# Kernel optimization log

Hardware: AMD Instinct MI355X
Metric: run time of the kernel (lower is better)

Reference implementation:

```python
import jax, jax.numpy as jnp
import numpy as np

N_NODES = 50000
E = 800000
D = 64
H = 128


def _ln(x, g, b, eps=1e-5):
    m = x.mean(-1, keepdims=True)
    v = ((x - m) ** 2).mean(-1, keepdims=True)
    return (x - m) * jax.lax.rsqrt(v + eps) * g + b


def setup_inputs() -> dict:
    key = jax.random.key(0)
    ks = jax.random.split(key, 8)
    return dict(
        node_emb=jax.random.normal(ks[0], (N_NODES, D), jnp.float32),
        src=jax.random.randint(ks[1], (E,), 0, N_NODES),
        dst=jax.random.randint(ks[2], (E,), 0, N_NODES),
        noise=jax.random.uniform(ks[3], (E,), jnp.float32, 1e-6, 1.0 - 1e-6),
        W1=jax.random.normal(ks[4], (2 * D, H), jnp.float32) * 0.05,
        b1=jnp.zeros((H,), jnp.float32),
        g1=jnp.ones((H,), jnp.float32),
        bt1=jnp.zeros((H,), jnp.float32),
        W2=jax.random.normal(ks[5], (H, H // 2), jnp.float32) * 0.05,
        b2=jnp.zeros((H // 2,), jnp.float32),
        g2=jnp.ones((H // 2,), jnp.float32),
        bt2=jnp.zeros((H // 2,), jnp.float32),
        W3=jax.random.normal(ks[6], (H // 2, 1), jnp.float32) * 0.05,
        b3=jnp.zeros((1,), jnp.float32),
    )


def reference(node_emb, src, dst, noise, W1, b1, g1, bt1, W2, b2, g2, bt2, W3, b3):
    # edge gather + concat: [E, 2D]
    edge_emb = jnp.concatenate([node_emb[src], node_emb[dst]], axis=1)
    # edge MLP with LayerNorm + relu (dropout=0 / eval)
    h = jax.nn.relu(_ln(edge_emb @ W1 + b1, g1, bt1))
    h = jax.nn.relu(_ln(h @ W2 + b2, g2, bt2))
    logit = (h @ W3 + b3).reshape(-1)  # [E]
    # concrete gate, bias=0, beta=1.0 (forward default)
    beta = 1.0
    gate = jax.nn.sigmoid((jnp.log(noise) - jnp.log1p(-noise) + logit) / beta)
    # degree norm: out_deg(src)^-1/2 * in_deg(dst)^-1/2, degrees clamped to >=1
    ones = jnp.ones((src.shape[0],), node_emb.dtype)
    out_deg = jnp.maximum(jax.ops.segment_sum(ones, src, num_segments=N_NODES), 1.0)
    in_deg = jnp.maximum(jax.ops.segment_sum(ones, dst, num_segments=N_NODES), 1.0)
    norm = jax.lax.rsqrt(out_deg)[src] * jax.lax.rsqrt(in_deg)[dst]
    return gate * norm
```

## Files before the change

kernel.cpp:

```cpp
#include <hip/hip_runtime.h>
#include <hip/hip_bf16.h>

#define N_NODES 50000
#define NE      800000
#define NT16    (NE / 16)
#define NTILES  (NE / 16)

typedef __attribute__((ext_vector_type(8)))  short bf16x8;
typedef __attribute__((ext_vector_type(4)))  float f32x4;
typedef __attribute__((ext_vector_type(4)))  int   i32x4;
typedef __attribute__((ext_vector_type(2)))  int   i32x2;

static __device__ __forceinline__ short f2bf(float x) {
    union { float f; unsigned u; } v; v.f = x;
    unsigned r = (v.u + 0x7fffu + ((v.u >> 16) & 1u)) >> 16;
    return (short)r;
}
static __device__ __forceinline__ float bflo(unsigned u) {
    union { unsigned u; float f; } v; v.u = u << 16; return v.f;
}
static __device__ __forceinline__ float bfhi(unsigned u) {
    union { unsigned u; float f; } v; v.u = u & 0xffff0000u; return v.f;
}
static __device__ __forceinline__ unsigned pk2bf(float a, float b) {
    union { __hip_bfloat162 h; unsigned u; } v;
    float2 f; f.x = a; f.y = b;
    v.h = __float22bfloat162_rn(f);
    return v.u;
}

#define OFF_W2   32768
#define OFF_B1   49152
#define OFF_B2   49408
#define OFF_GT1  49536
#define OFF_GT2  50048
#define OFF_W3   50304
#define IMG_B    50432
#define IMG_V4   (IMG_B / 16)


__global__ void prep_hist(const float* __restrict__ emb,
                          const int* __restrict__ src, const int* __restrict__ dst,
                          const float* __restrict__ W1, const float* __restrict__ b1,
                          const float* __restrict__ g1, const float* __restrict__ bt1,
                          const float* __restrict__ W2, const float* __restrict__ b2,
                          const float* __restrict__ g2, const float* __restrict__ bt2,
                          const float* __restrict__ W3,
                          ushort* __restrict__ embB, char* __restrict__ img,
                          int* __restrict__ outd, int* __restrict__ ind)
{
    const int i0 = blockIdx.x * 256 + threadIdx.x;
    const int n  = gridDim.x * 256;

    for (int t = i0; t < (N_NODES * 64 / 8); t += n) {
        const f32x4* p = (const f32x4*)(emb + (size_t)t * 8);
        f32x4 a = p[0], b = p[1];
        unsigned u0 = pk2bf(a[0], a[1]);
        unsigned u1 = pk2bf(a[2], a[3]);
        unsigned u2 = pk2bf(b[0], b[1]);
        unsigned u3 = pk2bf(b[2], b[3]);
        i32x4 o = {(int)u0, (int)u1, (int)u2, (int)u3};
        *(i32x4*)(embB + (size_t)t * 8) = o;
    }
    for (int t = i0; t < NE / 4; t += n) {
        i32x4 s4 = ((const i32x4*)src)[t];
        i32x4 d4 = ((const i32x4*)dst)[t];
        atomicAdd(outd + s4[0], 1); atomicAdd(outd + s4[1], 1);
        atomicAdd(outd + s4[2], 1); atomicAdd(outd + s4[3], 1);
        atomicAdd(ind + d4[0], 1); atomicAdd(ind + d4[1], 1);
        atomicAdd(ind + d4[2], 1); atomicAdd(ind + d4[3], 1);
    }
    ushort* W1f = (ushort*)img;
    for (int t = i0; t < 16384; t += n) {
        int j = t & 7, lane = (t >> 3) & 63, f = t >> 9;
        int tt = f >> 2, ks = f & 3, g = lane >> 4, c = lane & 15;
        W1f[t] = f2bf(W1[(ks * 32 + g * 8 + j) * 128 + tt * 16 + c]);
    }
    ushort* W2f = (ushort*)(img + OFF_W2);
    for (int t = i0; t < 8192; t += n) {
        int j = t & 7, lane = (t >> 3) & 63, f = t >> 9;
        int t2 = f >> 2, ks = f & 3, g = lane >> 4, c = lane & 15;
        W2f[t] = f2bf(W2[(ks * 32 + g * 8 + j) * 64 + t2 * 16 + c]);
    }
    if (i0 < 128) ((ushort*)(img + OFF_B1))[i0] = f2bf(b1[i0]);
    if (i0 < 64)  ((ushort*)(img + OFF_B2))[i0] = f2bf(b2[i0]);
    if (i0 < 128)
        ((unsigned*)(img + OFF_GT1))[i0] =
            (unsigned)(ushort)f2bf(g1[i0]) | ((unsigned)(ushort)f2bf(bt1[i0]) << 16);
    if (i0 < 64) {
        ((unsigned*)(img + OFF_GT2))[i0] =
            (unsigned)(ushort)f2bf(g2[i0]) | ((unsigned)(ushort)f2bf(bt2[i0]) << 16);
        ((ushort*)(img + OFF_W3))[i0] = f2bf(W3[i0]);
    }
}


__global__ __launch_bounds__(256, 3) void edge_mlp16(
    const ushort* __restrict__ embB,
    const int*   __restrict__ src, const int* __restrict__ dst,
    const float* __restrict__ noise,
    const i32x4* __restrict__ WFimg,
    const float* __restrict__ b3p,
    const int* __restrict__ outd, const int* __restrict__ ind,
    float* __restrict__ out)
{
    __shared__ i32x4 ldsv[IMG_V4];
    char* ldsb = (char*)ldsv;

    const int tid = threadIdx.x;
    for (int i = tid; i < IMG_V4; i += 256) ldsv[i] = WFimg[i];
    __syncthreads();

    const int l = tid & 63;
    const int g = l >> 4;
    const int c = l & 15;

    const float b3v = b3p[0];

    bf16x8 bone = {};
    bone[0] = (g == 0) ? (short)0x3F80 : (short)0;

    const int addrA = (((g & 1) * 2) * 16 + c) * 4;
    const int addrB = addrA + 64;

    const int gw = blockIdx.x * 4 + (tid >> 6);
    const int nw = gridDim.x * 4;

    int sn, dn;
    bf16x8 fS0, fS1, fD0, fD1;
    {
        int t0 = (gw < NT16) ? gw : (NT16 - 1);
        int e0p = t0 * 16 + c;
        sn = src[e0p]; dn = dst[e0p];
        const ushort* sp = embB + (size_t)sn * 64;
        const ushort* dp = embB + (size_t)dn * 64;
        fS0 = *(const bf16x8*)(sp + g * 8);
        fS1 = *(const bf16x8*)(sp + 32 + g * 8);
        fD0 = *(const bf16x8*)(dp + g * 8);
        fD1 = *(const bf16x8*)(dp + 32 + g * 8);
    }

    for (int tile = gw; tile < NT16; tile += nw) {
        unsigned tz;
        asm volatile("v_mov_b32 %0, 0" : "=v"(tz));
        const char* ldz = ldsb + tz;

        const int e0 = tile * 16 + c;

        const int tn  = tile + nw;
        const int tcl = (tn < NT16) ? tn : tile;
        const int e0n = tcl * 16 + c;
        int snN = src[e0n];
        int dnN = dst[e0n];
        float nz = noise[e0];
        int odv = outd[sn];
        int idv = ind[dn];

        const ushort* W1z = (const ushort*)ldz;
        f32x4 acc1[8] = {};
#pragma unroll
        for (int ks = 0; ks < 4; ++ks) {
            bf16x8 bf = (ks == 0) ? fS0 : (ks == 1) ? fS1 : (ks == 2) ? fD0 : fD1;
#pragma unroll
            for (int t = 0; t < 8; ++t) {
                bf16x8 w = *(const bf16x8*)(W1z + (t * 4 + ks) * 512 + l * 8);
                acc1[t] = __builtin_amdgcn_mfma_f32_16x16x32_bf16(w, bf, acc1[t], 0, 0, 0);
            }
        }
        const ushort* b1z = (const ushort*)(ldz + OFF_B1);
#pragma unroll
        for (int t = 0; t < 8; ++t) {
            bf16x8 w = {};
            short bv = b1z[t * 16 + c];
            w[0] = (g == 0) ? bv : (short)0;
            acc1[t] = __builtin_amdgcn_mfma_f32_16x16x32_bf16(w, bone, acc1[t], 0, 0, 0);
        }

        float s0 = 0.f, s1 = 0.f, q0 = 0.f, q1 = 0.f;
#pragma unroll
        for (int t = 0; t < 8; ++t) {
            float v0 = acc1[t][0], v1 = acc1[t][1], v2 = acc1[t][2], v3 = acc1[t][3];
            s0 += v0 + v2; q0 = fmaf(v0, v0, fmaf(v2, v2, q0));
            s1 += v1 + v3; q1 = fmaf(v1, v1, fmaf(v3, v3, q1));
        }
        float s = s0 + s1, q = q0 + q1;
        s += __shfl_xor(s, 16); s += __shfl_xor(s, 32);
        q += __shfl_xor(q, 16); q += __shfl_xor(q, 32);
        const float mu = s * (1.0f / 128.0f);
        const float rs = rsqrtf(q * (1.0f / 128.0f) - mu * mu + 1e-5f);
        const float c0 = -mu * rs;

        unsigned pku[8][2];
#pragma unroll
        for (int t = 0; t < 8; ++t) {
            i32x4 pg = *(const i32x4*)(ldz + OFF_GT1 + t * 64 + g * 16);
            float y0, y1, y2, y3;
            {
                float w0 = fmaf(acc1[t][0], rs, c0);
                y0 = fmaxf(fmaf(w0, bflo((unsigned)pg[0]), bfhi((unsigned)pg[0])), 0.f);
                float w1 = fmaf(acc1[t][1], rs, c0);
                y1 = fmaxf(fmaf(w1, bflo((unsigned)pg[1]), bfhi((unsigned)pg[1])), 0.f);
                float w2 = fmaf(acc1[t][2], rs, c0);
                y2 = fmaxf(fmaf(w2, bflo((unsigned)pg[2]), bfhi((unsigned)pg[2])), 0.f);
                float w3 = fmaf(acc1[t][3], rs, c0);
                y3 = fmaxf(fmaf(w3, bflo((unsigned)pg[3]), bfhi((unsigned)pg[3])), 0.f);
            }
            pku[t][0] = pk2bf(y0, y1);
            pku[t][1] = pk2bf(y2, y3);
        }

        const ushort* W2z = (const ushort*)(ldz + OFF_W2);
        f32x4 acc2[4] = {};
#pragma unroll
        for (int ks = 0; ks < 4; ++ks) {
            int a0 = __builtin_amdgcn_ds_bpermute(addrA, (int)pku[2 * ks][0]);
            int b0 = __builtin_amdgcn_ds_bpermute(addrA, (int)pku[2 * ks + 1][0]);
            int a1 = __builtin_amdgcn_ds_bpermute(addrA, (int)pku[2 * ks][1]);
            int b1_ = __builtin_amdgcn_ds_bpermute(addrA, (int)pku[2 * ks + 1][1]);
            int a2 = __builtin_amdgcn_ds_bpermute(addrB, (int)pku[2 * ks][0]);
            int b2_ = __builtin_amdgcn_ds_bpermute(addrB, (int)pku[2 * ks + 1][0]);
            int a3 = __builtin_amdgcn_ds_bpermute(addrB, (int)pku[2 * ks][1]);
            int b3_ = __builtin_amdgcn_ds_bpermute(addrB, (int)pku[2 * ks + 1][1]);
            union { i32x4 i; bf16x8 b; } u;
            u.i[0] = (g & 2) ? b0 : a0;
            u.i[1] = (g & 2) ? b1_ : a1;
            u.i[2] = (g & 2) ? b2_ : a2;
            u.i[3] = (g & 2) ? b3_ : a3;
#pragma unroll
            for (int t2 = 0; t2 < 4; ++t2) {
                bf16x8 w = *(const bf16x8*)(W2z + (t2 * 4 + ks) * 512 + l * 8);
                acc2[t2] = __builtin_amdgcn_mfma_f32_16x16x32_bf16(w, u.b, acc2[t2], 0, 0, 0);
            }
        }
        const ushort* b2z = (const ushort*)(ldz + OFF_B2);
#pragma unroll
        for (int t2 = 0; t2 < 4; ++t2) {
            bf16x8 w = {};
            short bv = b2z[t2 * 16 + c];
            w[0] = (g == 0) ? bv : (short)0;
            acc2[t2] = __builtin_amdgcn_mfma_f32_16x16x32_bf16(w, bone, acc2[t2], 0, 0, 0);
        }

        {
            const ushort* spn = embB + (size_t)snN * 64;
            const ushort* dpn = embB + (size_t)dnN * 64;
            fS0 = *(const bf16x8*)(spn + g * 8);
            fS1 = *(const bf16x8*)(spn + 32 + g * 8);
            fD0 = *(const bf16x8*)(dpn + g * 8);
            fD1 = *(const bf16x8*)(dpn + 32 + g * 8);
        }

        float t0 = 0.f, t1 = 0.f, p0 = 0.f, p1 = 0.f;
#pragma unroll
        for (int t2 = 0; t2 < 4; ++t2) {
            float v0 = acc2[t2][0], v1 = acc2[t2][1], v2 = acc2[t2][2], v3 = acc2[t2][3];
            t0 += v0 + v2; p0 = fmaf(v0, v0, fmaf(v2, v2, p0));
            t1 += v1 + v3; p1 = fmaf(v1, v1, fmaf(v3, v3, p1));
        }
        float s2 = t0 + t1, q2 = p0 + p1;
        s2 += __shfl_xor(s2, 16); s2 += __shfl_xor(s2, 32);
        q2 += __shfl_xor(q2, 16); q2 += __shfl_xor(q2, 32);
        const float mu2 = s2 * (1.0f / 64.0f);
        const float rs2 = rsqrtf(q2 * (1.0f / 64.0f) - mu2 * mu2 + 1e-5f);
        const float c02 = -mu2 * rs2;

        float lg = 0.f;
#pragma unroll
        for (int t2 = 0; t2 < 4; ++t2) {
            i32x4 pg = *(const i32x4*)(ldz + OFF_GT2 + t2 * 64 + g * 16);
            i32x2 wq = *(const i32x2*)(ldz + OFF_W3 + t2 * 32 + g * 8);
#pragma unroll
            for (int r = 0; r < 4; ++r) {
                unsigned ug = (unsigned)pg[r];
                unsigned wu = (unsigned)wq[r >> 1];
                float w3v = (r & 1) ? bfhi(wu) : bflo(wu);
                float w = fmaf(acc2[t2][r], rs2, c02);
                float y = fmaxf(fmaf(w, bflo(ug), bfhi(ug)), 0.f);
                lg = fmaf(y, w3v, lg);
            }
        }
        lg += __shfl_xor(lg, 16);
        lg += __shfl_xor(lg, 32);
        lg += b3v;

        if (g == 0) {
            float z = __logf(nz) - log1pf(-nz) + lg;
            float gate = 1.0f / (1.0f + __expf(-z));
            int od = odv; if (od < 1) od = 1;
            int idg = idv; if (idg < 1) idg = 1;
            out[e0] = gate * (rsqrtf((float)od) * rsqrtf((float)idg));
        }

        sn = snN; dn = dnN;
    }
}


__global__ void degree_hist(const int* __restrict__ src, const int* __restrict__ dst,
                            int* __restrict__ outd, int* __restrict__ ind) {
    int i = blockIdx.x * 256 + threadIdx.x;
    if (i < NE) {
        atomicAdd(outd + src[i], 1);
        atomicAdd(ind + dst[i], 1);
    }
}

__global__ __launch_bounds__(256, 2) void edge_mlp_mfma(
    const float* __restrict__ emb,
    const int*   __restrict__ src, const int* __restrict__ dst,
    const float* __restrict__ noise,
    const float* __restrict__ W1, const float* __restrict__ b1,
    const float* __restrict__ g1, const float* __restrict__ bt1,
    const float* __restrict__ W2, const float* __restrict__ b2,
    const float* __restrict__ g2, const float* __restrict__ bt2,
    const float* __restrict__ W3, const float* __restrict__ b3,
    const int*   __restrict__ outd, const int* __restrict__ ind,
    float* __restrict__ out)
{
    __shared__ short lds[32768];
    const int tid = threadIdx.x;
    const int wid = tid >> 6;
    const int l   = tid & 63;
    const int g   = l >> 4;
    const int c   = l & 15;

    for (int i = tid; i < 16384; i += 256) {
        int j = i & 7, lane = (i >> 3) & 63, p = i >> 9;
        int ks = p >> 3, t = p & 7;
        int row = ks * 32 + (lane >> 4) * 8 + j;
        int col = t * 16 + (lane & 15);
        lds[i] = f2bf(W1[row * 128 + col]);
    }
    for (int i = tid; i < 8192; i += 256) {
        int j = i & 7, lane = (i >> 3) & 63, p = i >> 9;
        int ks = p >> 2, t = p & 3;
        int row = ks * 32 + (lane >> 4) * 8 + j;
        int col = t * 16 + (lane & 15);
        lds[16384 + i] = f2bf(W2[row * 64 + col]);
    }
    __syncthreads();

    short* Hl = lds + 24576 + wid * 2048;
    float b1v[8], g1v[8], t1v[8];
#pragma unroll
    for (int t = 0; t < 8; ++t) { int f = t * 16 + c; b1v[t] = b1[f]; g1v[t] = g1[f]; t1v[t] = bt1[f]; }
    float b2v[4], g2v[4], t2v[4], w3v[4];
#pragma unroll
    for (int t = 0; t < 4; ++t) { int f = t * 16 + c; b2v[t] = b2[f]; g2v[t] = g2[f]; t2v[t] = bt2[f]; w3v[t] = W3[f]; }
    const float b3v = b3[0];

    const int gw = blockIdx.x * 4 + wid;
    const int nw = gridDim.x * 4;

    for (int tile = gw; tile < NTILES; tile += nw) {
        const int e0 = tile * 16 + c;
        const int sn = src[e0], dn = dst[e0];
        const f32x4* sp = (const f32x4*)(emb + (size_t)sn * 64);
        const f32x4* dp = (const f32x4*)(emb + (size_t)dn * 64);
        f32x4 u[8];
        u[0] = sp[2 * g]; u[1] = sp[2 * g + 1];
        u[2] = sp[8 + 2 * g]; u[3] = sp[8 + 2 * g + 1];
        u[4] = dp[2 * g]; u[5] = dp[2 * g + 1];
        u[6] = dp[8 + 2 * g]; u[7] = dp[8 + 2 * g + 1];

        bf16x8 a1[4];
#pragma unroll
        for (int ks = 0; ks < 4; ++ks) {
            f32x4 x0 = u[2 * ks], x1 = u[2 * ks + 1];
            bf16x8 a;
            a[0] = f2bf(x0[0]); a[1] = f2bf(x0[1]); a[2] = f2bf(x0[2]); a[3] = f2bf(x0[3]);
            a[4] = f2bf(x1[0]); a[5] = f2bf(x1[1]); a[6] = f2bf(x1[2]); a[7] = f2bf(x1[3]);
            a1[ks] = a;
        }
        f32x4 acc1[8];
#pragma unroll
        for (int t = 0; t < 8; ++t) { f32x4 z = {b1v[t], b1v[t], b1v[t], b1v[t]}; acc1[t] = z; }
#pragma unroll
        for (int ks = 0; ks < 4; ++ks) {
#pragma unroll
            for (int t = 0; t < 8; ++t) {
                bf16x8 b = *(const bf16x8*)(lds + (ks * 8 + t) * 512 + l * 8);
                acc1[t] = __builtin_amdgcn_mfma_f32_16x16x32_bf16(a1[ks], b, acc1[t], 0, 0, 0);
            }
        }
        float mean[4], rstd[4];
#pragma unroll
        for (int r = 0; r < 4; ++r) {
            float s = acc1[0][r];
#pragma unroll
            for (int t = 1; t < 8; ++t) s += acc1[t][r];
            s += __shfl_xor(s, 1); s += __shfl_xor(s, 2);
            s += __shfl_xor(s, 4); s += __shfl_xor(s, 8);
            float m = s * (1.0f / 128.0f);
            float q = 0.f;
#pragma unroll
            for (int t = 0; t < 8; ++t) { float d = acc1[t][r] - m; q = fmaf(d, d, q); }
            q += __shfl_xor(q, 1); q += __shfl_xor(q, 2);
            q += __shfl_xor(q, 4); q += __shfl_xor(q, 8);
            mean[r] = m; rstd[r] = rsqrtf(q * (1.0f / 128.0f) + 1e-5f);
        }
#pragma unroll
        for (int r = 0; r < 4; ++r) {
            int rw = g * 4 + r;
            int swz = (rw & 7) << 3;
#pragma unroll
            for (int t = 0; t < 8; ++t) {
                float y = fmaf((acc1[t][r] - mean[r]) * rstd[r], g1v[t], t1v[t]);
                y = fmaxf(y, 0.f);
                Hl[rw * 128 + ((t * 16 + c) ^ swz)] = f2bf(y);
            }
        }
        bf16x8 a2[4];
        const int swzr = (c & 7) << 3;
#pragma unroll
        for (int ks = 0; ks < 4; ++ks)
            a2[ks] = *(const bf16x8*)(Hl + c * 128 + ((ks * 32 + g * 8) ^ swzr));

        f32x4 acc2[4];
#pragma unroll
        for (int t = 0; t < 4; ++t) { f32x4 z = {b2v[t], b2v[t], b2v[t], b2v[t]}; acc2[t] = z; }
#pragma unroll
        for (int ks = 0; ks < 4; ++ks) {
#pragma unroll
            for (int t = 0; t < 4; ++t) {
                bf16x8 b = *(const bf16x8*)(lds + 16384 + (ks * 4 + t) * 512 + l * 8);
                acc2[t] = __builtin_amdgcn_mfma_f32_16x16x32_bf16(a2[ks], b, acc2[t], 0, 0, 0);
            }
        }
        float logit[4];
#pragma unroll
        for (int r = 0; r < 4; ++r) {
            float s = acc2[0][r] + acc2[1][r] + acc2[2][r] + acc2[3][r];
            s += __shfl_xor(s, 1); s += __shfl_xor(s, 2);
            s += __shfl_xor(s, 4); s += __shfl_xor(s, 8);
            float m = s * (1.0f / 64.0f);
            float q = 0.f;
#pragma unroll
            for (int t = 0; t < 4; ++t) { float d = acc2[t][r] - m; q = fmaf(d, d, q); }
            q += __shfl_xor(q, 1); q += __shfl_xor(q, 2);
            q += __shfl_xor(q, 4); q += __shfl_xor(q, 8);
            float rs = rsqrtf(q * (1.0f / 64.0f) + 1e-5f);
            float p = 0.f;
#pragma unroll
            for (int t = 0; t < 4; ++t) {
                float y = fmaf((acc2[t][r] - m) * rs, g2v[t], t2v[t]);
                y = fmaxf(y, 0.f);
                p = fmaf(y, w3v[t], p);
            }
            p += __shfl_xor(p, 1); p += __shfl_xor(p, 2);
            p += __shfl_xor(p, 4); p += __shfl_xor(p, 8);
            logit[r] = p + b3v;
        }
        if (c < 4) {
            int e = tile * 16 + g * 4 + c;
            float lg = (c == 0) ? logit[0] : (c == 1) ? logit[1] : (c == 2) ? logit[2] : logit[3];
            float nz = noise[e];
            float z = __logf(nz) - log1pf(-nz) + lg;
            float gate = 1.0f / (1.0f + __expf(-z));
            int od = outd[src[e]]; if (od < 1) od = 1;
            int idg = ind[dst[e]]; if (idg < 1) idg = 1;
            out[e] = gate * (rsqrtf((float)od) * rsqrtf((float)idg));
        }
    }
}


extern "C" void kernel_launch(void* const* d_in, const int* in_sizes, int n_in,
                              void* d_out, int out_size, void* d_ws, size_t ws_size,
                              hipStream_t stream) {
    const float* emb   = (const float*)d_in[0];
    const int*   src   = (const int*)  d_in[1];
    const int*   dst   = (const int*)  d_in[2];
    const float* noise = (const float*)d_in[3];
    const float* W1  = (const float*)d_in[4];
    const float* b1  = (const float*)d_in[5];
    const float* g1  = (const float*)d_in[6];
    const float* bt1 = (const float*)d_in[7];
    const float* W2  = (const float*)d_in[8];
    const float* b2  = (const float*)d_in[9];
    const float* g2  = (const float*)d_in[10];
    const float* bt2 = (const float*)d_in[11];
    const float* W3  = (const float*)d_in[12];
    const float* b3  = (const float*)d_in[13];

    char* ws = (char*)d_ws;
    const size_t NEED = 6400000 + IMG_B + 400000;

    if (ws_size >= NEED) {
        ushort* embB = (ushort*)ws;
        char*   img  = ws + 6400000;
        int* outd = (int*)(ws + 6400000 + IMG_B);
        int* ind  = outd + N_NODES;

        hipMemsetAsync(outd, 0, 2 * N_NODES * sizeof(int), stream);
        prep_hist<<<2048, 256, 0, stream>>>(emb, src, dst, W1, b1, g1, bt1,
                                            W2, b2, g2, bt2, W3,
                                            embB, img, outd, ind);
        edge_mlp16<<<1536, 256, 0, stream>>>(embB, src, dst, noise, (const i32x4*)img,
                                             b3, outd, ind, (float*)d_out);
    } else {
        int* outd = (int*)ws;
        int* ind  = outd + N_NODES;
        hipMemsetAsync(outd, 0, 2 * N_NODES * sizeof(int), stream);
        degree_hist<<<(NE + 255) / 256, 256, 0, stream>>>(src, dst, outd, ind);
        edge_mlp_mfma<<<512, 256, 0, stream>>>(emb, src, dst, noise,
                                               W1, b1, g1, bt1,
                                               W2, b2, g2, bt2,
                                               W3, b3, outd, ind,
                                               (float*)d_out);
    }
}
```

Measured before the change: 172.2 us.

## Precompute per-node first-layer projections and gather them per edge

Splits the first linear layer algebraically: each node's embedding is projected once by the source and destination halves of W1 in a new node-level MFMA GEMM kernel, with half the bias folded into each half. The edge kernel then gathers two 128-wide bf16 projection rows per edge and adds them, replacing the per-edge 128x128 matmul. The ds_bpermute shuffle is also replaced with xor shuffles. This removes most of the edge-level first-layer MFMA work and shrinks the LDS image to raise occupancy, but per-edge gather traffic roughly doubles (512 bytes per edge instead of 256) and a separate kernel launch plus a 25.6 MB intermediate buffer are added.

New measurement: 188.3 us. 9.4% more time.

```diff
diff --git a/kernel.cpp b/kernel.cpp
--- a/kernel.cpp
+++ b/kernel.cpp
@@ -8,6 +8,7 @@
 
 typedef __attribute__((ext_vector_type(8)))  short bf16x8;
 typedef __attribute__((ext_vector_type(4)))  float f32x4;
+typedef __attribute__((ext_vector_type(16))) float f32x16;
 typedef __attribute__((ext_vector_type(4)))  int   i32x4;
 typedef __attribute__((ext_vector_type(2)))  int   i32x2;
 
@@ -29,39 +30,38 @@
     return v.u;
 }
 
-#define OFF_W2   32768
-#define OFF_B1   49152
-#define OFF_B2   49408
-#define OFF_GT1  49536
-#define OFF_GT2  50048
-#define OFF_W3   50304
-#define IMG_B    50432
-#define IMG_V4   (IMG_B / 16)
-
-
-__global__ void prep_hist(const float* __restrict__ emb,
-                          const int* __restrict__ src, const int* __restrict__ dst,
-                          const float* __restrict__ W1, const float* __restrict__ b1,
-                          const float* __restrict__ g1, const float* __restrict__ bt1,
-                          const float* __restrict__ W2, const float* __restrict__ b2,
-                          const float* __restrict__ g2, const float* __restrict__ bt2,
-                          const float* __restrict__ W3,
-                          ushort* __restrict__ embB, char* __restrict__ img,
-                          int* __restrict__ outd, int* __restrict__ ind)
+#define GOFF_BH  32768
+#define GIMG_B   33280
+#define GIMG_V4  (GIMG_B / 16)
+
+#define I2_B2    16384
+#define I2_GT1   16512
+#define I2_GT2   17024
+#define I2_W3    17280
+#define IMG2_B   17408
+#define IMG2_V4  (IMG2_B / 16)
+
+#define WS_P     0
+#define WS_GIMG  25600000
+#define WS_IMG2  25633280
+#define WS_OUTD  25650688
+#define WS_IND   25850688
+#define WS_NEED  26050688
+
+
+__global__ void prep_all(const float* __restrict__ emb,
+                         const int* __restrict__ src, const int* __restrict__ dst,
+                         const float* __restrict__ W1, const float* __restrict__ b1,
+                         const float* __restrict__ g1, const float* __restrict__ bt1,
+                         const float* __restrict__ W2, const float* __restrict__ b2,
+                         const float* __restrict__ g2, const float* __restrict__ bt2,
+                         const float* __restrict__ W3,
+                         char* __restrict__ gimg, char* __restrict__ img2,
+                         int* __restrict__ outd, int* __restrict__ ind)
 {
     const int i0 = blockIdx.x * 256 + threadIdx.x;
     const int n  = gridDim.x * 256;
 
-    for (int t = i0; t < (N_NODES * 64 / 8); t += n) {
-        const f32x4* p = (const f32x4*)(emb + (size_t)t * 8);
-        f32x4 a = p[0], b = p[1];
-        unsigned u0 = pk2bf(a[0], a[1]);
-        unsigned u1 = pk2bf(a[2], a[3]);
-        unsigned u2 = pk2bf(b[0], b[1]);
-        unsigned u3 = pk2bf(b[2], b[3]);
-        i32x4 o = {(int)u0, (int)u1, (int)u2, (int)u3};
-        *(i32x4*)(embB + (size_t)t * 8) = o;
-    }
     for (int t = i0; t < NE / 4; t += n) {
         i32x4 s4 = ((const i32x4*)src)[t];
         i32x4 d4 = ((const i32x4*)dst)[t];
@@ -70,45 +70,117 @@
         atomicAdd(ind + d4[0], 1); atomicAdd(ind + d4[1], 1);
         atomicAdd(ind + d4[2], 1); atomicAdd(ind + d4[3], 1);
     }
-    ushort* W1f = (ushort*)img;
+    ushort* W1f = (ushort*)gimg;
     for (int t = i0; t < 16384; t += n) {
         int j = t & 7, lane = (t >> 3) & 63, f = t >> 9;
-        int tt = f >> 2, ks = f & 3, g = lane >> 4, c = lane & 15;
-        W1f[t] = f2bf(W1[(ks * 32 + g * 8 + j) * 128 + tt * 16 + c]);
-    }
-    ushort* W2f = (ushort*)(img + OFF_W2);
+        int ft = f >> 2, ks = f & 3, h = lane >> 5, cc = lane & 31;
+        int k = 16 * ks + 8 * h + j;
+        int fo = 32 * ft + cc;
+        float v = (fo < 128) ? W1[k * 128 + fo] : W1[(64 + k) * 128 + (fo - 128)];
+        W1f[t] = f2bf(v);
+    }
+    if (i0 < 256) ((ushort*)(gimg + GOFF_BH))[i0] = f2bf(0.5f * b1[i0 & 127]);
+
+    ushort* W2f = (ushort*)img2;
     for (int t = i0; t < 8192; t += n) {
         int j = t & 7, lane = (t >> 3) & 63, f = t >> 9;
         int t2 = f >> 2, ks = f & 3, g = lane >> 4, c = lane & 15;
         W2f[t] = f2bf(W2[(ks * 32 + g * 8 + j) * 64 + t2 * 16 + c]);
     }
-    if (i0 < 128) ((ushort*)(img + OFF_B1))[i0] = f2bf(b1[i0]);
-    if (i0 < 64)  ((ushort*)(img + OFF_B2))[i0] = f2bf(b2[i0]);
+    if (i0 < 64)  ((ushort*)(img2 + I2_B2))[i0] = f2bf(b2[i0]);
     if (i0 < 128)
-        ((unsigned*)(img + OFF_GT1))[i0] =
+        ((unsigned*)(img2 + I2_GT1))[i0] =
             (unsigned)(ushort)f2bf(g1[i0]) | ((unsigned)(ushort)f2bf(bt1[i0]) << 16);
     if (i0 < 64) {
-        ((unsigned*)(img + OFF_GT2))[i0] =
+        ((unsigned*)(img2 + I2_GT2))[i0] =
             (unsigned)(ushort)f2bf(g2[i0]) | ((unsigned)(ushort)f2bf(bt2[i0]) << 16);
-        ((ushort*)(img + OFF_W3))[i0] = f2bf(W3[i0]);
-    }
-}
-
-
-__global__ __launch_bounds__(256, 3) void edge_mlp16(
-    const ushort* __restrict__ embB,
+        ((ushort*)(img2 + I2_W3))[i0] = f2bf(W3[i0]);
+    }
+}
+
+
+#define NT_NODE 1563
+
+__global__ __launch_bounds__(256, 2) void gemm_P(
+    const float* __restrict__ emb, const i32x4* __restrict__ GIMG,
+    ushort* __restrict__ P)
+{
+    __shared__ i32x4 ldsg[GIMG_V4];
+    char* gb = (char*)ldsg;
+    const int tid = threadIdx.x;
+    for (int i = tid; i < GIMG_V4; i += 256) ldsg[i] = GIMG[i];
+    __syncthreads();
+
+    const int l = tid & 63;
+    const int h = l >> 5;
+    const int c = l & 31;
+
+    bf16x8 bone = {};
+    bone[0] = (h == 0) ? (short)0x3F80 : (short)0;
+
+    const ushort* W1z = (const ushort*)gb;
+    const ushort* bhz = (const ushort*)(gb + GOFF_BH);
+
+    const int gw = blockIdx.x * 4 + (tid >> 6);
+    const int nw = gridDim.x * 4;
+    const int NTT = NT_NODE * 8;
+
+    for (int tt = gw; tt < NTT; tt += nw) {
+        const int nt = tt >> 3;
+        const int ft = tt & 7;
+        const int nn = nt * 32 + c;
+        const int ncl = (nn < N_NODES) ? nn : (N_NODES - 1);
+        const float* er = emb + (size_t)ncl * 64;
+
+        f32x16 acc = {};
+#pragma unroll
+        for (int ks = 0; ks < 4; ++ks) {
+            f32x4 x0 = *(const f32x4*)(er + 16 * ks + 8 * h);
+            f32x4 x1 = *(const f32x4*)(er + 16 * ks + 8 * h + 4);
+            bf16x8 bf;
+            bf[0] = f2bf(x0[0]); bf[1] = f2bf(x0[1]); bf[2] = f2bf(x0[2]); bf[3] = f2bf(x0[3]);
+            bf[4] = f2bf(x1[0]); bf[5] = f2bf(x1[1]); bf[6] = f2bf(x1[2]); bf[7] = f2bf(x1[3]);
+            bf16x8 w = *(const bf16x8*)(W1z + (ft * 4 + ks) * 512 + l * 8);
+            acc = __builtin_amdgcn_mfma_f32_32x32x16_bf16(w, bf, acc, 0, 0, 0);
+        }
+        {
+            bf16x8 w = {};
+            short bv = (short)bhz[32 * ft + c];
+            w[0] = (h == 0) ? bv : (short)0;
+            acc = __builtin_amdgcn_mfma_f32_32x32x16_bf16(w, bone, acc, 0, 0, 0);
+        }
+        if (nn < N_NODES) {
+#pragma unroll
+            for (int q = 0; q < 4; ++q) {
+                int fl = 8 * q + 4 * h;
+                int f  = 32 * ft + fl;
+                int fh = f & 127, half = f >> 7;
+                int t  = fh >> 4, gg = (fh >> 2) & 3;
+                ushort* dp = P + (size_t)nn * 256 + half * 128 + gg * 32 + t * 4;
+                i32x2 o;
+                o[0] = (int)pk2bf(acc[4 * q],     acc[4 * q + 1]);
+                o[1] = (int)pk2bf(acc[4 * q + 2], acc[4 * q + 3]);
+                *(i32x2*)dp = o;
+            }
+        }
+    }
+}
+
+
+__global__ __launch_bounds__(256, 4) void edge_mlp_p(
+    const ushort* __restrict__ P,
     const int*   __restrict__ src, const int* __restrict__ dst,
     const float* __restrict__ noise,
-    const i32x4* __restrict__ WFimg,
+    const i32x4* __restrict__ IMG2,
     const float* __restrict__ b3p,
     const int* __restrict__ outd, const int* __restrict__ ind,
     float* __restrict__ out)
 {
-    __shared__ i32x4 ldsv[IMG_V4];
+    __shared__ i32x4 ldsv[IMG2_V4];
     char* ldsb = (char*)ldsv;
 
     const int tid = threadIdx.x;
-    for (int i = tid; i < IMG_V4; i += 256) ldsv[i] = WFimg[i];
+    for (int i = tid; i < IMG2_V4; i += 256) ldsv[i] = IMG2[i];
     __syncthreads();
 
     const int l = tid & 63;
@@ -120,24 +192,19 @@
     bf16x8 bone = {};
     bone[0] = (g == 0) ? (short)0x3F80 : (short)0;
 
-    const int addrA = (((g & 1) * 2) * 16 + c) * 4;
-    const int addrB = addrA + 64;
-
     const int gw = blockIdx.x * 4 + (tid >> 6);
     const int nw = gridDim.x * 4;
 
     int sn, dn;
-    bf16x8 fS0, fS1, fD0, fD1;
+    i32x4 ps0, ps1, ps2, ps3, pd0, pd1, pd2, pd3;
     {
         int t0 = (gw < NT16) ? gw : (NT16 - 1);
         int e0p = t0 * 16 + c;
         sn = src[e0p]; dn = dst[e0p];
-        const ushort* sp = embB + (size_t)sn * 64;
-        const ushort* dp = embB + (size_t)dn * 64;
-        fS0 = *(const bf16x8*)(sp + g * 8);
-        fS1 = *(const bf16x8*)(sp + 32 + g * 8);
-        fD0 = *(const bf16x8*)(dp + g * 8);
-        fD1 = *(const bf16x8*)(dp + 32 + g * 8);
+        const i32x4* sp = (const i32x4*)(P + (size_t)sn * 256 + g * 32);
+        const i32x4* dp = (const i32x4*)(P + (size_t)dn * 256 + 128 + g * 32);
+        ps0 = sp[0]; ps1 = sp[1]; ps2 = sp[2]; ps3 = sp[3];
+        pd0 = dp[0]; pd1 = dp[1]; pd2 = dp[2]; pd3 = dp[3];
     }
 
     for (int tile = gw; tile < NT16; tile += nw) {
@@ -156,34 +223,22 @@
         int odv = outd[sn];
         int idv = ind[dn];
 
-        const ushort* W1z = (const ushort*)ldz;
-        f32x4 acc1[8] = {};
-#pragma unroll
-        for (int ks = 0; ks < 4; ++ks) {
-            bf16x8 bf = (ks == 0) ? fS0 : (ks == 1) ? fS1 : (ks == 2) ? fD0 : fD1;
-#pragma unroll
-            for (int t = 0; t < 8; ++t) {
-                bf16x8 w = *(const bf16x8*)(W1z + (t * 4 + ks) * 512 + l * 8);
-                acc1[t] = __builtin_amdgcn_mfma_f32_16x16x32_bf16(w, bf, acc1[t], 0, 0, 0);
-            }
-        }
-        const ushort* b1z = (const ushort*)(ldz + OFF_B1);
-#pragma unroll
-        for (int t = 0; t < 8; ++t) {
-            bf16x8 w = {};
-            short bv = b1z[t * 16 + c];
-            w[0] = (g == 0) ? bv : (short)0;
-            acc1[t] = __builtin_amdgcn_mfma_f32_16x16x32_bf16(w, bone, acc1[t], 0, 0, 0);
-        }
-
-        float s0 = 0.f, s1 = 0.f, q0 = 0.f, q1 = 0.f;
-#pragma unroll
-        for (int t = 0; t < 8; ++t) {
-            float v0 = acc1[t][0], v1 = acc1[t][1], v2 = acc1[t][2], v3 = acc1[t][3];
-            s0 += v0 + v2; q0 = fmaf(v0, v0, fmaf(v2, v2, q0));
-            s1 += v1 + v3; q1 = fmaf(v1, v1, fmaf(v3, v3, q1));
-        }
-        float s = s0 + s1, q = q0 + q1;
+        float s = 0.f, q = 0.f;
+        {
+            i32x4 pcs[4] = {ps0, ps1, ps2, ps3};
+            i32x4 pcd[4] = {pd0, pd1, pd2, pd3};
+#pragma unroll
+            for (int i = 0; i < 4; ++i) {
+#pragma unroll
+                for (int w = 0; w < 4; ++w) {
+                    unsigned sv = (unsigned)pcs[i][w], dv = (unsigned)pcd[i][w];
+                    float a = bflo(sv) + bflo(dv);
+                    float b = bfhi(sv) + bfhi(dv);
+                    s += a + b;
+                    q = fmaf(a, a, fmaf(b, b, q));
+                }
+            }
+        }
         s += __shfl_xor(s, 16); s += __shfl_xor(s, 32);
         q += __shfl_xor(q, 16); q += __shfl_xor(q, 32);
         const float mu = s * (1.0f / 128.0f);
@@ -191,73 +246,80 @@
         const float c0 = -mu * rs;
 
         unsigned pku[8][2];
-#pragma unroll
-        for (int t = 0; t < 8; ++t) {
-            i32x4 pg = *(const i32x4*)(ldz + OFF_GT1 + t * 64 + g * 16);
-            float y0, y1, y2, y3;
-            {
-                float w0 = fmaf(acc1[t][0], rs, c0);
-                y0 = fmaxf(fmaf(w0, bflo((unsigned)pg[0]), bfhi((unsigned)pg[0])), 0.f);
-                float w1 = fmaf(acc1[t][1], rs, c0);
-                y1 = fmaxf(fmaf(w1, bflo((unsigned)pg[1]), bfhi((unsigned)pg[1])), 0.f);
-                float w2 = fmaf(acc1[t][2], rs, c0);
-                y2 = fmaxf(fmaf(w2, bflo((unsigned)pg[2]), bfhi((unsigned)pg[2])), 0.f);
-                float w3 = fmaf(acc1[t][3], rs, c0);
-                y3 = fmaxf(fmaf(w3, bflo((unsigned)pg[3]), bfhi((unsigned)pg[3])), 0.f);
-            }
-            pku[t][0] = pk2bf(y0, y1);
-            pku[t][1] = pk2bf(y2, y3);
-        }
-
-        const ushort* W2z = (const ushort*)(ldz + OFF_W2);
+        {
+            i32x4 pcs[4] = {ps0, ps1, ps2, ps3};
+            i32x4 pcd[4] = {pd0, pd1, pd2, pd3};
+#pragma unroll
+            for (int t = 0; t < 8; ++t) {
+                i32x4 pg = *(const i32x4*)(ldz + I2_GT1 + t * 64 + g * 16);
+                unsigned sv0 = (unsigned)pcs[t >> 1][(t & 1) * 2];
+                unsigned sv1 = (unsigned)pcs[t >> 1][(t & 1) * 2 + 1];
+                unsigned dv0 = (unsigned)pcd[t >> 1][(t & 1) * 2];
+                unsigned dv1 = (unsigned)pcd[t >> 1][(t & 1) * 2 + 1];
+                float h0 = bflo(sv0) + bflo(dv0);
+                float h1_ = bfhi(sv0) + bfhi(dv0);
+                float h2 = bflo(sv1) + bflo(dv1);
+                float h3 = bfhi(sv1) + bfhi(dv1);
+                float y0 = fmaxf(fmaf(fmaf(h0, rs, c0), bflo((unsigned)pg[0]), bfhi((unsigned)pg[0])), 0.f);
+                float y1 = fmaxf(fmaf(fmaf(h1_, rs, c0), bflo((unsigned)pg[1]), bfhi((unsigned)pg[1])), 0.f);
+                float y2 = fmaxf(fmaf(fmaf(h2, rs, c0), bflo((unsigned)pg[2]), bfhi((unsigned)pg[2])), 0.f);
+                float y3 = fmaxf(fmaf(fmaf(h3, rs, c0), bflo((unsigned)pg[3]), bfhi((unsigned)pg[3])), 0.f);
+                pku[t][0] = pk2bf(y0, y1);
+                pku[t][1] = pk2bf(y2, y3);
+            }
+        }
+
+        {
+            const i32x4* sp = (const i32x4*)(P + (size_t)snN * 256 + g * 32);
+            const i32x4* dp = (const i32x4*)(P + (size_t)dnN * 256 + 128 + g * 32);
+            ps0 = sp[0]; ps1 = sp[1]; ps2 = sp[2]; ps3 = sp[3];
+            pd0 = dp[0]; pd1 = dp[1]; pd2 = dp[2]; pd3 = dp[3];
+        }
+
+        const ushort* W2z = (const ushort*)ldz;
         f32x4 acc2[4] = {};
+        const bool gh = (g & 2) != 0;
+        const bool g0 = (g & 1) != 0;
 #pragma unroll
         for (int ks = 0; ks < 4; ++ks) {
-            int a0 = __builtin_amdgcn_ds_bpermute(addrA, (int)pku[2 * ks][0]);
-            int b0 = __builtin_amdgcn_ds_bpermute(addrA, (int)pku[2 * ks + 1][0]);
-            int a1 = __builtin_amdgcn_ds_bpermute(addrA, (int)pku[2 * ks][1]);
-            int b1_ = __builtin_amdgcn_ds_bpermute(addrA, (int)pku[2 * ks + 1][1]);
-            int a2 = __builtin_amdgcn_ds_bpermute(addrB, (int)pku[2 * ks][0]);
-            int b2_ = __builtin_amdgcn_ds_bpermute(addrB, (int)pku[2 * ks + 1][0]);
-            int a3 = __builtin_amdgcn_ds_bpermute(addrB, (int)pku[2 * ks][1]);
-            int b3_ = __builtin_amdgcn_ds_bpermute(addrB, (int)pku[2 * ks + 1][1]);
+            unsigned o0 = pku[2 * ks][0],     o1 = pku[2 * ks][1];
+            unsigned p0 = pku[2 * ks + 1][0], p1 = pku[2 * ks + 1][1];
+            unsigned s16_0 = gh ? p0 : o0, s16_1 = gh ? p1 : o1;
+            unsigned r16_0 = (unsigned)__shfl_xor((int)s16_0, 16);
+            unsigned r16_1 = (unsigned)__shfl_xor((int)s16_1, 16);
+            unsigned s32_0 = gh ? o0 : p0, s32_1 = gh ? o1 : p1;
+            unsigned r32_0 = (unsigned)__shfl_xor((int)s32_0, 32);
+            unsigned r32_1 = (unsigned)__shfl_xor((int)s32_1, 32);
+            unsigned r48_0 = (unsigned)__shfl_xor((int)s32_0, 48);
+            unsigned r48_1 = (unsigned)__shfl_xor((int)s32_1, 48);
             union { i32x4 i; bf16x8 b; } u;
-            u.i[0] = (g & 2) ? b0 : a0;
-            u.i[1] = (g & 2) ? b1_ : a1;
-            u.i[2] = (g & 2) ? b2_ : a2;
-            u.i[3] = (g & 2) ? b3_ : a3;
+            u.i[0] = (int)(g0 ? (gh ? r16_0 : r48_0) : (gh ? r32_0 : o0));
+            u.i[1] = (int)(g0 ? (gh ? r16_1 : r48_1) : (gh ? r32_1 : o1));
+            u.i[2] = (int)(g0 ? (gh ? p0 : r32_0) : (gh ? r48_0 : r16_0));
+            u.i[3] = (int)(g0 ? (gh ? p1 : r32_1) : (gh ? r48_1 : r16_1));
 #pragma unroll
             for (int t2 = 0; t2 < 4; ++t2) {
                 bf16x8 w = *(const bf16x8*)(W2z + (t2 * 4 + ks) * 512 + l * 8);
                 acc2[t2] = __builtin_amdgcn_mfma_f32_16x16x32_bf16(w, u.b, acc2[t2], 0, 0, 0);
             }
         }
-        const ushort* b2z = (const ushort*)(ldz + OFF_B2);
+        const ushort* b2z = (const ushort*)(ldz + I2_B2);
 #pragma unroll
         for (int t2 = 0; t2 < 4; ++t2) {
             bf16x8 w = {};
-            short bv = b2z[t2 * 16 + c];
+            short bv = (short)b2z[t2 * 16 + c];
             w[0] = (g == 0) ? bv : (short)0;
             acc2[t2] = __builtin_amdgcn_mfma_f32_16x16x32_bf16(w, bone, acc2[t2], 0, 0, 0);
         }
 
-        {
-            const ushort* spn = embB + (size_t)snN * 64;
-            const ushort* dpn = embB + (size_t)dnN * 64;
-            fS0 = *(const bf16x8*)(spn + g * 8);
-            fS1 = *(const bf16x8*)(spn + 32 + g * 8);
-            fD0 = *(const bf16x8*)(dpn + g * 8);
-            fD1 = *(const bf16x8*)(dpn + 32 + g * 8);
-        }
-
-        float t0 = 0.f, t1 = 0.f, p0 = 0.f, p1 = 0.f;
+        float t0 = 0.f, t1 = 0.f, p0s = 0.f, p1s = 0.f;
 #pragma unroll
         for (int t2 = 0; t2 < 4; ++t2) {
             float v0 = acc2[t2][0], v1 = acc2[t2][1], v2 = acc2[t2][2], v3 = acc2[t2][3];
-            t0 += v0 + v2; p0 = fmaf(v0, v0, fmaf(v2, v2, p0));
-            t1 += v1 + v3; p1 = fmaf(v1, v1, fmaf(v3, v3, p1));
-        }
-        float s2 = t0 + t1, q2 = p0 + p1;
+            t0 += v0 + v2; p0s = fmaf(v0, v0, fmaf(v2, v2, p0s));
+            t1 += v1 + v3; p1s = fmaf(v1, v1, fmaf(v3, v3, p1s));
+        }
+        float s2 = t0 + t1, q2 = p0s + p1s;
         s2 += __shfl_xor(s2, 16); s2 += __shfl_xor(s2, 32);
         q2 += __shfl_xor(q2, 16); q2 += __shfl_xor(q2, 32);
         const float mu2 = s2 * (1.0f / 64.0f);
@@ -267,8 +329,8 @@
         float lg = 0.f;
 #pragma unroll
         for (int t2 = 0; t2 < 4; ++t2) {
-            i32x4 pg = *(const i32x4*)(ldz + OFF_GT2 + t2 * 64 + g * 16);
-            i32x2 wq = *(const i32x2*)(ldz + OFF_W3 + t2 * 32 + g * 8);
+            i32x4 pg = *(const i32x4*)(ldz + I2_GT2 + t2 * 64 + g * 16);
+            i32x2 wq = *(const i32x2*)(ldz + I2_W3 + t2 * 32 + g * 8);
 #pragma unroll
             for (int r = 0; r < 4; ++r) {
                 unsigned ug = (unsigned)pg[r];
@@ -484,19 +546,20 @@
     const float* b3  = (const float*)d_in[13];
 
     char* ws = (char*)d_ws;
-    const size_t NEED = 6400000 + IMG_B + 400000;
-
-    if (ws_size >= NEED) {
-        ushort* embB = (ushort*)ws;
-        char*   img  = ws + 6400000;
-        int* outd = (int*)(ws + 6400000 + IMG_B);
-        int* ind  = outd + N_NODES;
+
+    if (ws_size >= (size_t)WS_NEED) {
+        ushort* P    = (ushort*)(ws + WS_P);
+        char*   gimg = ws + WS_GIMG;
+        char*   img2 = ws + WS_IMG2;
+        int* outd = (int*)(ws + WS_OUTD);
+        int* ind  = (int*)(ws + WS_IND);
 
         hipMemsetAsync(outd, 0, 2 * N_NODES * sizeof(int), stream);
-        prep_hist<<<2048, 256, 0, stream>>>(emb, src, dst, W1, b1, g1, bt1,
-                                            W2, b2, g2, bt2, W3,
-                                            embB, img, outd, ind);
-        edge_mlp16<<<1536, 256, 0, stream>>>(embB, src, dst, noise, (const i32x4*)img,
+        prep_all<<<1024, 256, 0, stream>>>(emb, src, dst, W1, b1, g1, bt1,
+                                           W2, b2, g2, bt2, W3,
+                                           gimg, img2, outd, ind);
+        gemm_P<<<1024, 256, 0, stream>>>(emb, (const i32x4*)gimg, P);
+        edge_mlp_p<<<2048, 256, 0, stream>>>(P, src, dst, noise, (const i32x4*)img2,
                                              b3, outd, ind, (float*)d_out);
     } else {
         int* outd = (int*)ws;
```
